# Optimization experiments

Measured on AMD Instinct MI355X. Metric: run time of the kernel, lower is better.

The kernel has to match this reference:

```python
import jax, jax.numpy as jnp
import numpy as np


def setup_inputs() -> dict:
    key = jax.random.key(0)
    k1, k2, k3 = jax.random.split(key, 3)
    seq_len, input_size, hidden_size = 8192, 2048, 2048
    inputs = jax.random.normal(k1, (seq_len, input_size), dtype=jnp.float32)
    W_xh = jax.random.normal(k2, (hidden_size, input_size), dtype=jnp.float32) * 0.01
    W_hh = jax.random.normal(k3, (hidden_size, hidden_size), dtype=jnp.float32) * 0.01
    b_h = jnp.zeros((hidden_size, 1), dtype=jnp.float32)
    return {"inputs": inputs, "W_xh": W_xh, "W_hh": W_hh, "b_h": b_h}


def reference(inputs, W_xh, W_hh, b_h):
    # h_t = tanh(W_xh @ x_t + W_hh @ h_{t-1} + b_h), h_0 = 0
    # Torch code uses column vectors (hidden,1); we use flat (hidden,) vectors,
    # which is the same math.
    b = b_h[:, 0]
    h0 = jnp.zeros((W_hh.shape[0],), dtype=inputs.dtype)

    def step(h_prev, x_t):
        h_t = jnp.tanh(W_xh @ x_t + W_hh @ h_prev + b)
        return h_t, h_t

    h_T, outputs = jax.lax.scan(step, h0, inputs)
    # outputs: (seq_len, hidden)  == stacked list of h_t; h_T == final state
    return outputs, h_T
```

## Files before the change

kernel.cpp:

```cpp
#include <hip/hip_runtime.h>
#include <math.h>

#define H 2048
#define S 8192
#define RPB 8
#define NBLK (H / RPB)
#define PW (H / 2)
#define WPT (PW / 256)

__global__ __launch_bounds__(256) void gemm_xw(const float* __restrict__ X,
                                               const float* __restrict__ W,
                                               float* __restrict__ U) {
    __shared__ float As[16][64];
    __shared__ float Bs[16][64];
    const int tid = threadIdx.x;
    const int t0 = blockIdx.x * 64;
    const int j0 = blockIdx.y * 64;
    const int tx = tid & 15, ty = tid >> 4;

    float acc[4][4] = {};
    const int lr = tid >> 2;
    const int lk = (tid & 3) * 4;

    for (int k0 = 0; k0 < H; k0 += 16) {
        float4 a = *(const float4*)&X[(size_t)(t0 + lr) * H + k0 + lk];
        float4 b = *(const float4*)&W[(size_t)(j0 + lr) * H + k0 + lk];
        As[lk + 0][lr] = a.x; As[lk + 1][lr] = a.y; As[lk + 2][lr] = a.z; As[lk + 3][lr] = a.w;
        Bs[lk + 0][lr] = b.x; Bs[lk + 1][lr] = b.y; Bs[lk + 2][lr] = b.z; Bs[lk + 3][lr] = b.w;
        __syncthreads();
#pragma unroll
        for (int kk = 0; kk < 16; ++kk) {
            float4 av = *(const float4*)&As[kk][ty * 4];
            float4 bv = *(const float4*)&Bs[kk][tx * 4];
            float aa[4] = {av.x, av.y, av.z, av.w};
            float bb[4] = {bv.x, bv.y, bv.z, bv.w};
#pragma unroll
            for (int i = 0; i < 4; ++i)
#pragma unroll
                for (int j = 0; j < 4; ++j)
                    acc[i][j] += aa[i] * bb[j];
        }
        __syncthreads();
    }
#pragma unroll
    for (int i = 0; i < 4; ++i) {
        float4 v = {acc[i][0], acc[i][1], acc[i][2], acc[i][3]};
        *(float4*)&U[(size_t)(t0 + ty * 4 + i) * H + j0 + tx * 4] = v;
    }
}

__global__ void init_ws(unsigned long long* __restrict__ hvt) {
    int i = blockIdx.x * blockDim.x + threadIdx.x;
    if (i < PW) hvt[i] = 0ull;
    else if (i < 2 * PW) hvt[i] = 0x0000000100000001ull;
}

__global__ __launch_bounds__(256) void rnn_recur(float* __restrict__ out,
                                                 const float* __restrict__ Whh,
                                                 const float* __restrict__ bias,
                                                 unsigned long long* __restrict__ hvt) {
    __shared__ float red[2][RPB][4];
    const int tid = threadIdx.x;
    const int r0 = blockIdx.x * RPB;
    const int lane = tid & 63;
    const int wid = tid >> 6;

    float2 wv[RPB][WPT];
#pragma unroll
    for (int j = 0; j < RPB; ++j)
#pragma unroll
        for (int i = 0; i < WPT; ++i)
            wv[j][i] = *(const float2*)&Whh[(size_t)(r0 + j) * H + 2 * (i * 256 + tid)];

    const float bb = bias[r0 + (tid & 7)];

    for (int t = 0; t < S; ++t) {
        float u_val = out[(size_t)t * H + r0 + (tid & 7)];

        const unsigned int ep = ((unsigned int)t >> 1) & 1u;
        const unsigned long long* hb = &hvt[(size_t)(t & 1) * PW];
        float acc[RPB] = {};
        unsigned int pend = (1u << WPT) - 1u;
        while (pend) {
            unsigned long long vv[WPT];
#pragma unroll
            for (int i = 0; i < WPT; ++i)
                if (pend & (1u << i))
                    vv[i] = __hip_atomic_load(&hb[i * 256 + tid], __ATOMIC_RELAXED,
                                              __HIP_MEMORY_SCOPE_AGENT);
#pragma unroll
            for (int i = 0; i < WPT; ++i)
                if (pend & (1u << i)) {
                    const unsigned int blo = (unsigned int)vv[i];
                    const unsigned int bhi = (unsigned int)(vv[i] >> 32);
                    if ((((blo ^ ep) | (bhi ^ ep)) & 1u) == 0u) {
                        const float fl = __uint_as_float(blo);
                        const float fh = __uint_as_float(bhi);
#pragma unroll
                        for (int j = 0; j < RPB; ++j)
                            acc[j] += wv[j][i].x * fl + wv[j][i].y * fh;
                        pend &= ~(1u << i);
                    }
                }
            if (pend) __builtin_amdgcn_s_sleep(1);
        }

#pragma unroll
        for (int j = 0; j < RPB; ++j) {
#pragma unroll
            for (int m = 32; m; m >>= 1)
                acc[j] += __shfl_xor(acc[j], m, 64);
        }
        if (lane < RPB) red[t & 1][lane][wid] = acc[lane];
        __syncthreads();

        if (tid < RPB) {
            const float4 r4 = *(const float4*)red[t & 1][tid];
            const float val = tanhf(r4.x + r4.y + r4.z + r4.w + u_val + bb);
            out[(size_t)t * H + r0 + tid] = val;
            if (t == S - 1) out[(size_t)S * H + r0 + tid] = val;
            const float pv = __shfl_xor(val, 1, 64);
            if ((tid & 1) == 0) {
                const unsigned int e2 = (((unsigned int)(t + 1)) >> 1) & 1u;
                const unsigned long long pk =
                    ((unsigned long long)((__float_as_uint(pv) & ~1u) | e2) << 32) |
                    (unsigned long long)((__float_as_uint(val) & ~1u) | e2);
                __hip_atomic_store(&hvt[(size_t)((t + 1) & 1) * PW + (r0 >> 1) + (tid >> 1)],
                                   pk, __ATOMIC_RELAXED, __HIP_MEMORY_SCOPE_AGENT);
            }
        }
    }
}

extern "C" void kernel_launch(void* const* d_in, const int* in_sizes, int n_in,
                              void* d_out, int out_size, void* d_ws, size_t ws_size,
                              hipStream_t stream) {
    const float* X    = (const float*)d_in[0];
    const float* Wxh  = (const float*)d_in[1];
    const float* Whh  = (const float*)d_in[2];
    const float* bias = (const float*)d_in[3];
    float* out = (float*)d_out;
    unsigned long long* hvt = (unsigned long long*)d_ws;

    init_ws<<<(2 * PW + 255) / 256, 256, 0, stream>>>(hvt);

    dim3 ggrid(S / 64, H / 64);
    gemm_xw<<<ggrid, 256, 0, stream>>>(X, Wxh, out);

    void* args[] = {(void*)&out, (void*)&Whh, (void*)&bias, (void*)&hvt};
    hipLaunchCooperativeKernel((void*)rnn_recur, dim3(NBLK), dim3(256), args, 0, stream);
}
```

Baseline: 23.69 ms.

## Widen hidden-state exchange to 16-byte packets with replicated buffers and transpose reduction

The per-step hidden-state broadcast is changed from 8-byte atomic packets to 16-byte packets, loaded and stored with sc1 inline-assembly dwordx4 instructions. Each packet carries four floats tagged by the epoch bit, so every thread now polls two locations per step instead of four. The state buffer is written twice, and odd and even blocks poll different copies, to spread contention on the polled lines. The cross-lane reduction becomes a transpose-style butterfly that uses fewer shuffles. A fallback path with 8-byte atomic loads is added in case the 16-byte loads are not observed as a single unit (torn reads), which adds complexity and relies on dwordx4 stores becoming visible as a unit.

```diff
diff --git a/kernel.cpp b/kernel.cpp
--- a/kernel.cpp
+++ b/kernel.cpp
@@ -5,8 +5,11 @@
 #define S 8192
 #define RPB 8
 #define NBLK (H / RPB)
-#define PW (H / 2)
-#define WPT (PW / 256)
+#define PW16 (H / 4)
+#define NREP 2
+
+typedef float f32x4 __attribute__((ext_vector_type(4)));
+typedef unsigned int u32x4 __attribute__((ext_vector_type(4)));
 
 __global__ __launch_bounds__(256) void gemm_xw(const float* __restrict__ X,
                                                const float* __restrict__ W,
@@ -49,56 +52,110 @@
     }
 }
 
-__global__ void init_ws(unsigned long long* __restrict__ hvt) {
+__global__ void init_ws(unsigned int* __restrict__ w) {
     int i = blockIdx.x * blockDim.x + threadIdx.x;
-    if (i < PW) hvt[i] = 0ull;
-    else if (i < 2 * PW) hvt[i] = 0x0000000100000001ull;
+    if (i < NREP * 2 * PW16 * 4) w[i] = (i >> 11) & 1u;
+}
+
+__device__ inline u32x4 ld16_sc1(const void* p) {
+    u32x4 r;
+    asm volatile("global_load_dwordx4 %0, %1, off sc1\n\t"
+                 "s_waitcnt vmcnt(0)"
+                 : "=&v"(r) : "v"(p) : "memory");
+    return r;
+}
+__device__ inline void ld16x2_sc1(const void* p0, const void* p1, u32x4& a, u32x4& b) {
+    asm volatile("global_load_dwordx4 %0, %2, off sc1\n\t"
+                 "global_load_dwordx4 %1, %3, off sc1\n\t"
+                 "s_waitcnt vmcnt(0)"
+                 : "=&v"(a), "=&v"(b) : "v"(p0), "v"(p1) : "memory");
+}
+__device__ inline void st16_sc1(void* p, u32x4 v) {
+    asm volatile("global_store_dwordx4 %0, %1, off sc1" :: "v"(p), "v"(v) : "memory");
 }
 
 __global__ __launch_bounds__(256) void rnn_recur(float* __restrict__ out,
                                                  const float* __restrict__ Whh,
                                                  const float* __restrict__ bias,
                                                  unsigned long long* __restrict__ hvt) {
-    __shared__ float red[2][RPB][4];
+    __shared__ __align__(16) float red[2][RPB][4];
     const int tid = threadIdx.x;
     const int r0 = blockIdx.x * RPB;
     const int lane = tid & 63;
     const int wid = tid >> 6;
 
-    float2 wv[RPB][WPT];
+    float4 wv[RPB][2];
 #pragma unroll
     for (int j = 0; j < RPB; ++j)
 #pragma unroll
-        for (int i = 0; i < WPT; ++i)
-            wv[j][i] = *(const float2*)&Whh[(size_t)(r0 + j) * H + 2 * (i * 256 + tid)];
+        for (int i = 0; i < 2; ++i)
+            wv[j][i] = *(const float4*)&Whh[(size_t)(r0 + j) * H + 4 * (i * 256 + tid)];
 
     const float bb = bias[r0 + (tid & 7)];
+    f32x4* const hbase = (f32x4*)hvt;
+    int fb = 0;
 
     for (int t = 0; t < S; ++t) {
         float u_val = out[(size_t)t * H + r0 + (tid & 7)];
 
         const unsigned int ep = ((unsigned int)t >> 1) & 1u;
-        const unsigned long long* hb = &hvt[(size_t)(t & 1) * PW];
+        const f32x4* hb = hbase + (size_t)(blockIdx.x & 1) * (2 * PW16) +
+                          (size_t)(t & 1) * PW16;
         float acc[RPB] = {};
-        unsigned int pend = (1u << WPT) - 1u;
+        unsigned int pend = 3u;
+        int spin = 0;
+
+        while (pend && !fb) {
+            u32x4 va, vb;
+            if (pend == 3u)      ld16x2_sc1(hb + tid, hb + 256 + tid, va, vb);
+            else if (pend == 1u) va = ld16_sc1(hb + tid);
+            else                 vb = ld16_sc1(hb + 256 + tid);
+            if (pend & 1u) {
+                if ((((va.x ^ ep) | (va.y ^ ep) | (va.z ^ ep) | (va.w ^ ep)) & 1u) == 0u) {
+                    const float h0 = __uint_as_float(va.x), h1 = __uint_as_float(va.y);
+                    const float h2 = __uint_as_float(va.z), h3 = __uint_as_float(va.w);
+#pragma unroll
+                    for (int j = 0; j < RPB; ++j)
+                        acc[j] += wv[j][0].x * h0 + wv[j][0].y * h1 +
+                                  wv[j][0].z * h2 + wv[j][0].w * h3;
+                    pend &= ~1u;
+                }
+            }
+            if (pend & 2u) {
+                if ((((vb.x ^ ep) | (vb.y ^ ep) | (vb.z ^ ep) | (vb.w ^ ep)) & 1u) == 0u) {
+                    const float h0 = __uint_as_float(vb.x), h1 = __uint_as_float(vb.y);
+                    const float h2 = __uint_as_float(vb.z), h3 = __uint_as_float(vb.w);
+#pragma unroll
+                    for (int j = 0; j < RPB; ++j)
+                        acc[j] += wv[j][1].x * h0 + wv[j][1].y * h1 +
+                                  wv[j][1].z * h2 + wv[j][1].w * h3;
+                    pend &= ~2u;
+                }
+            }
+            if (pend) {
+                __builtin_amdgcn_s_sleep(1);
+                if (++spin > 512) fb = 1;
+            }
+        }
         while (pend) {
-            unsigned long long vv[WPT];
-#pragma unroll
-            for (int i = 0; i < WPT; ++i)
-                if (pend & (1u << i))
-                    vv[i] = __hip_atomic_load(&hb[i * 256 + tid], __ATOMIC_RELAXED,
-                                              __HIP_MEMORY_SCOPE_AGENT);
-#pragma unroll
-            for (int i = 0; i < WPT; ++i)
+#pragma unroll
+            for (int i = 0; i < 2; ++i)
                 if (pend & (1u << i)) {
-                    const unsigned int blo = (unsigned int)vv[i];
-                    const unsigned int bhi = (unsigned int)(vv[i] >> 32);
-                    if ((((blo ^ ep) | (bhi ^ ep)) & 1u) == 0u) {
-                        const float fl = __uint_as_float(blo);
-                        const float fh = __uint_as_float(bhi);
+                    const unsigned long long* q =
+                        (const unsigned long long*)(hb + i * 256 + tid);
+                    unsigned long long lo = __hip_atomic_load(q, __ATOMIC_RELAXED,
+                                                              __HIP_MEMORY_SCOPE_AGENT);
+                    unsigned long long hi = __hip_atomic_load(q + 1, __ATOMIC_RELAXED,
+                                                              __HIP_MEMORY_SCOPE_AGENT);
+                    u32x4 v; v.x = (unsigned int)lo; v.y = (unsigned int)(lo >> 32);
+                    v.z = (unsigned int)hi; v.w = (unsigned int)(hi >> 32);
+                    if ((((v.x ^ ep) | (v.y ^ ep) | (v.z ^ ep) | (v.w ^ ep)) & 1u) == 0u) {
+                        const float h0 = __uint_as_float(v.x), h1 = __uint_as_float(v.y);
+                        const float h2 = __uint_as_float(v.z), h3 = __uint_as_float(v.w);
 #pragma unroll
                         for (int j = 0; j < RPB; ++j)
-                            acc[j] += wv[j][i].x * fl + wv[j][i].y * fh;
+                            acc[j] += wv[j][i].x * h0 + wv[j][i].y * h1 +
+                                      wv[j][i].z * h2 + wv[j][i].w * h3;
                         pend &= ~(1u << i);
                     }
                 }
@@ -106,27 +163,50 @@
         }
 
 #pragma unroll
-        for (int j = 0; j < RPB; ++j) {
-#pragma unroll
-            for (int m = 32; m; m >>= 1)
-                acc[j] += __shfl_xor(acc[j], m, 64);
-        }
-        if (lane < RPB) red[t & 1][lane][wid] = acc[lane];
+        for (int j = 0; j < 4; ++j) {
+            float s = (lane & 1) ? acc[j] : acc[j + 4];
+            float r = __shfl_xor(s, 1, 64);
+            acc[j] = ((lane & 1) ? acc[j + 4] : acc[j]) + r;
+        }
+#pragma unroll
+        for (int j = 0; j < 2; ++j) {
+            float s = (lane & 2) ? acc[j] : acc[j + 2];
+            float r = __shfl_xor(s, 2, 64);
+            acc[j] = ((lane & 2) ? acc[j + 2] : acc[j]) + r;
+        }
+        {
+            float s = (lane & 4) ? acc[0] : acc[1];
+            float r = __shfl_xor(s, 4, 64);
+            acc[0] = ((lane & 4) ? acc[1] : acc[0]) + r;
+        }
+#pragma unroll
+        for (int m = 8; m <= 32; m <<= 1)
+            acc[0] += __shfl_xor(acc[0], m, 64);
+        if (lane < 8)
+            red[t & 1][((lane & 1) << 2) | (lane & 2) | ((lane & 4) >> 2)][wid] = acc[0];
         __syncthreads();
 
-        if (tid < RPB) {
+        if (tid < 8) {
             const float4 r4 = *(const float4*)red[t & 1][tid];
             const float val = tanhf(r4.x + r4.y + r4.z + r4.w + u_val + bb);
             out[(size_t)t * H + r0 + tid] = val;
             if (t == S - 1) out[(size_t)S * H + r0 + tid] = val;
-            const float pv = __shfl_xor(val, 1, 64);
-            if ((tid & 1) == 0) {
+            const float p0 = __shfl(val, (int)(tid & 4) | 0, 64);
+            const float p1 = __shfl(val, (int)(tid & 4) | 1, 64);
+            const float p2 = __shfl(val, (int)(tid & 4) | 2, 64);
+            const float p3 = __shfl(val, (int)(tid & 4) | 3, 64);
+            if ((tid & 3) == 0) {
                 const unsigned int e2 = (((unsigned int)(t + 1)) >> 1) & 1u;
-                const unsigned long long pk =
-                    ((unsigned long long)((__float_as_uint(pv) & ~1u) | e2) << 32) |
-                    (unsigned long long)((__float_as_uint(val) & ~1u) | e2);
-                __hip_atomic_store(&hvt[(size_t)((t + 1) & 1) * PW + (r0 >> 1) + (tid >> 1)],
-                                   pk, __ATOMIC_RELAXED, __HIP_MEMORY_SCOPE_AGENT);
+                u32x4 pk;
+                pk.x = (__float_as_uint(p0) & ~1u) | e2;
+                pk.y = (__float_as_uint(p1) & ~1u) | e2;
+                pk.z = (__float_as_uint(p2) & ~1u) | e2;
+                pk.w = (__float_as_uint(p3) & ~1u) | e2;
+                const int widx = (r0 >> 2) + (tid >> 2);
+                const size_t par = (size_t)((t + 1) & 1) * PW16;
+#pragma unroll
+                for (int rep = 0; rep < NREP; ++rep)
+                    st16_sc1(hbase + (size_t)rep * (2 * PW16) + par + widx, pk);
             }
         }
     }
@@ -142,7 +222,7 @@
     float* out = (float*)d_out;
     unsigned long long* hvt = (unsigned long long*)d_ws;
 
-    init_ws<<<(2 * PW + 255) / 256, 256, 0, stream>>>(hvt);
+    init_ws<<<(NREP * 2 * PW16 * 4 + 255) / 256, 256, 0, stream>>>((unsigned int*)hvt);
 
     dim3 ggrid(S / 64, H / 64);
     gemm_xw<<<ggrid, 256, 0, stream>>>(X, Wxh, out);
```

Result: no change. 23.76 ms (+0.3%).

## Use 16 rows per block, replicated h buffers and 16-byte sc1 polling

Applied to the files above, without the earlier changes.

Doubles rows per block to 16, which halves the block count to 128 and gives each thread 8 contiguous h values. Each thread polls two 16-byte chunks with inline global_load_dwordx4 sc1 instead of 64-bit atomics. The flag scheme becomes a 2-bit epoch packed into float LSBs. The hidden-state exchange buffer is written twice (NREP=2), and odd and even blocks poll different copies to spread contention. A transpose-style butterfly shuffle cuts shuffle count for the 16-row reduction. The aim is lower per-step synchronisation latency, at the cost of more register pressure, hand-written cache-policy assembly, and the sleep in the spin loop being removed.

```diff
diff --git a/kernel.cpp b/kernel.cpp
--- a/kernel.cpp
+++ b/kernel.cpp
@@ -3,10 +3,12 @@
 
 #define H 2048
 #define S 8192
-#define RPB 8
+#define RPB 16
 #define NBLK (H / RPB)
-#define PW (H / 2)
-#define WPT (PW / 256)
+#define PARBYTES (H * 4)
+#define NREP 2
+
+typedef unsigned int u32x4 __attribute__((ext_vector_type(4)));
 
 __global__ __launch_bounds__(256) void gemm_xw(const float* __restrict__ X,
                                                const float* __restrict__ W,
@@ -49,85 +51,132 @@
     }
 }
 
-__global__ void init_ws(unsigned long long* __restrict__ hvt) {
+__global__ void init_ws(unsigned long long* __restrict__ w) {
     int i = blockIdx.x * blockDim.x + threadIdx.x;
-    if (i < PW) hvt[i] = 0ull;
-    else if (i < 2 * PW) hvt[i] = 0x0000000100000001ull;
+    if (i < NREP * 2 * (PARBYTES / 8))
+        w[i] = ((i >> 10) & 1) ? 0x0000000100000001ull : 0ull;
+}
+
+__device__ inline void poll2(const void* pc, u32x4& c0, u32x4& c1) {
+    asm volatile(
+        "global_load_dwordx4 %0, %2, off sc1\n\t"
+        "global_load_dwordx4 %1, %2, off offset:16 sc1\n\t"
+        "s_waitcnt vmcnt(0)"
+        : "=&v"(c0), "=&v"(c1)
+        : "v"(pc)
+        : "memory");
+}
+__device__ inline void st16_sc1(void* p, u32x4 v) {
+    asm volatile("global_store_dwordx4 %0, %1, off sc1" :: "v"(p), "v"(v) : "memory");
 }
 
 __global__ __launch_bounds__(256) void rnn_recur(float* __restrict__ out,
                                                  const float* __restrict__ Whh,
                                                  const float* __restrict__ bias,
                                                  unsigned long long* __restrict__ hvt) {
-    __shared__ float red[2][RPB][4];
-    const int tid = threadIdx.x;
-    const int r0 = blockIdx.x * RPB;
+    __shared__ float part[2][4][RPB];
+    const int tid  = threadIdx.x;
     const int lane = tid & 63;
-    const int wid = tid >> 6;
-
-    float2 wv[RPB][WPT];
+    const int wid  = tid >> 6;
+    const int r0   = blockIdx.x * RPB;
+
+    float4 wv[RPB][2];
 #pragma unroll
     for (int j = 0; j < RPB; ++j)
 #pragma unroll
-        for (int i = 0; i < WPT; ++i)
-            wv[j][i] = *(const float2*)&Whh[(size_t)(r0 + j) * H + 2 * (i * 256 + tid)];
-
-    const float bb = bias[r0 + (tid & 7)];
+        for (int i = 0; i < 2; ++i)
+            wv[j][i] = *(const float4*)&Whh[(size_t)(r0 + j) * H + 8 * tid + 4 * i];
+
+    const float bb = bias[r0 + (tid & 15)];
+    char* const hrep = (char*)hvt + (size_t)(blockIdx.x & 1) * (2 * PARBYTES);
 
     for (int t = 0; t < S; ++t) {
-        float u_val = out[(size_t)t * H + r0 + (tid & 7)];
-
-        const unsigned int ep = ((unsigned int)t >> 1) & 1u;
-        const unsigned long long* hb = &hvt[(size_t)(t & 1) * PW];
+        float u_val = out[(size_t)t * H + r0 + (tid & 15)];
+
+        const unsigned int e  = ((unsigned int)t >> 1) & 3u;
+        const unsigned int e0 = e & 1u, e1 = (e >> 1) & 1u;
+        const char* pc = hrep + (size_t)(t & 1) * PARBYTES + tid * 32;
+
         float acc[RPB] = {};
-        unsigned int pend = (1u << WPT) - 1u;
+        unsigned int pend = 3u;
         while (pend) {
-            unsigned long long vv[WPT];
-#pragma unroll
-            for (int i = 0; i < WPT; ++i)
-                if (pend & (1u << i))
-                    vv[i] = __hip_atomic_load(&hb[i * 256 + tid], __ATOMIC_RELAXED,
-                                              __HIP_MEMORY_SCOPE_AGENT);
-#pragma unroll
-            for (int i = 0; i < WPT; ++i)
+            u32x4 c0, c1;
+            poll2(pc, c0, c1);
+#pragma unroll
+            for (int i = 0; i < 2; ++i) {
                 if (pend & (1u << i)) {
-                    const unsigned int blo = (unsigned int)vv[i];
-                    const unsigned int bhi = (unsigned int)(vv[i] >> 32);
-                    if ((((blo ^ ep) | (bhi ^ ep)) & 1u) == 0u) {
-                        const float fl = __uint_as_float(blo);
-                        const float fh = __uint_as_float(bhi);
+                    const u32x4 v = i ? c1 : c0;
+                    if ((((v.x ^ e0) | (v.z ^ e0) | (v.y ^ e1) | (v.w ^ e1)) & 1u) == 0u) {
+                        const float h0 = __uint_as_float(v.x), h1 = __uint_as_float(v.y);
+                        const float h2 = __uint_as_float(v.z), h3 = __uint_as_float(v.w);
 #pragma unroll
                         for (int j = 0; j < RPB; ++j)
-                            acc[j] += wv[j][i].x * fl + wv[j][i].y * fh;
+                            acc[j] += wv[j][i].x * h0 + wv[j][i].y * h1 +
+                                      wv[j][i].z * h2 + wv[j][i].w * h3;
                         pend &= ~(1u << i);
                     }
                 }
-            if (pend) __builtin_amdgcn_s_sleep(1);
-        }
-
-#pragma unroll
-        for (int j = 0; j < RPB; ++j) {
-#pragma unroll
-            for (int m = 32; m; m >>= 1)
-                acc[j] += __shfl_xor(acc[j], m, 64);
-        }
-        if (lane < RPB) red[t & 1][lane][wid] = acc[lane];
+            }
+        }
+
+#pragma unroll
+        for (int j = 0; j < 8; ++j) {
+            float s = (lane & 1) ? acc[j] : acc[j + 8];
+            float r = __shfl_xor(s, 1, 64);
+            acc[j] = ((lane & 1) ? acc[j + 8] : acc[j]) + r;
+        }
+#pragma unroll
+        for (int j = 0; j < 4; ++j) {
+            float s = (lane & 2) ? acc[j] : acc[j + 4];
+            float r = __shfl_xor(s, 2, 64);
+            acc[j] = ((lane & 2) ? acc[j + 4] : acc[j]) + r;
+        }
+#pragma unroll
+        for (int j = 0; j < 2; ++j) {
+            float s = (lane & 4) ? acc[j] : acc[j + 2];
+            float r = __shfl_xor(s, 4, 64);
+            acc[j] = ((lane & 4) ? acc[j + 2] : acc[j]) + r;
+        }
+        {
+            float s = (lane & 8) ? acc[0] : acc[1];
+            float r = __shfl_xor(s, 8, 64);
+            acc[0] = ((lane & 8) ? acc[1] : acc[0]) + r;
+        }
+        acc[0] += __shfl_xor(acc[0], 16, 64);
+        acc[0] += __shfl_xor(acc[0], 32, 64);
+
+        if (lane < 16) {
+            const int row = ((lane & 1) << 3) | ((lane & 2) << 1) |
+                            ((lane & 4) >> 1) | ((lane & 8) >> 3);
+            part[t & 1][wid][row] = acc[0];
+        }
         __syncthreads();
 
         if (tid < RPB) {
-            const float4 r4 = *(const float4*)red[t & 1][tid];
-            const float val = tanhf(r4.x + r4.y + r4.z + r4.w + u_val + bb);
+            const float sum = part[t & 1][0][tid] + part[t & 1][1][tid] +
+                              part[t & 1][2][tid] + part[t & 1][3][tid];
+            const float val = tanhf(sum + u_val + bb);
+            const float s0 = __shfl(val, (tid & 12) | 0, 64);
+            const float s1 = __shfl(val, (tid & 12) | 1, 64);
+            const float s2 = __shfl(val, (tid & 12) | 2, 64);
+            const float s3 = __shfl(val, (tid & 12) | 3, 64);
+            if ((tid & 3) == 0) {
+                const unsigned int ee  = (((unsigned int)(t + 1)) >> 1) & 3u;
+                const unsigned int ee0 = ee & 1u, ee1 = (ee >> 1) & 1u;
+                u32x4 pk;
+                pk.x = (__float_as_uint(s0) & ~1u) | ee0;
+                pk.y = (__float_as_uint(s1) & ~1u) | ee1;
+                pk.z = (__float_as_uint(s2) & ~1u) | ee0;
+                pk.w = (__float_as_uint(s3) & ~1u) | ee1;
+                char* dst = (char*)hvt + (size_t)((t + 1) & 1) * PARBYTES +
+                            (size_t)(r0 + tid) * 4;
+                asm volatile("s_waitcnt vmcnt(0)" ::: "memory");
+#pragma unroll
+                for (int rep = 0; rep < NREP; ++rep)
+                    st16_sc1(dst + (size_t)rep * (2 * PARBYTES), pk);
+            }
             out[(size_t)t * H + r0 + tid] = val;
             if (t == S - 1) out[(size_t)S * H + r0 + tid] = val;
-            const float pv = __shfl_xor(val, 1, 64);
-            if ((tid & 1) == 0) {
-                const unsigned int e2 = (((unsigned int)(t + 1)) >> 1) & 1u;
-                const unsigned long long pk =
-                    ((unsigned long long)((__float_as_uint(pv) & ~1u) | e2) << 32) |
-                    (unsigned long long)((__float_as_uint(val) & ~1u) | e2);
-                __hip_atomic_store(&hvt[(size_t)((t + 1) & 1) * PW + (r0 >> 1) + (tid >> 1)],
-                                   pk, __ATOMIC_RELAXED, __HIP_MEMORY_SCOPE_AGENT);
-            }
         }
     }
 }
@@ -142,7 +191,7 @@
     float* out = (float*)d_out;
     unsigned long long* hvt = (unsigned long long*)d_ws;
 
-    init_ws<<<(2 * PW + 255) / 256, 256, 0, stream>>>(hvt);
+    init_ws<<<(NREP * 2 * (PARBYTES / 8) + 255) / 256, 256, 0, stream>>>(hvt);
 
     dim3 ggrid(S / 64, H / 64);
     gemm_xw<<<ggrid, 256, 0, stream>>>(X, Wxh, out);
```

After: 19.65 ms (median of 2 runs). 17.1% less time.
